# Optimization experiments

Measured on AMD Instinct MI355X. Metric: run time of the kernel, lower is better.

## Reference

```python
import jax, jax.numpy as jnp
import numpy as np

B, T, DIM = 64, 4096, 256
NFILT, KSIZE = 32, 31
PAD = (KSIZE - 1) // 2
NEG = -1e30  # score mask value (finite stand-in for -inf, safe for grads)


def setup_inputs() -> dict:
    key = jax.random.key(0)
    ks = jax.random.split(key, 10)
    query = jax.random.normal(ks[0], (B, DIM), dtype=jnp.float32)
    keys = jax.random.normal(ks[1], (B, T, DIM), dtype=jnp.float32)
    values = jax.random.normal(ks[2], (B, T, DIM), dtype=jnp.float32)
    prev_alignment = jax.random.uniform(ks[3], (B, T), dtype=jnp.float32)
    prev_alignment = prev_alignment / jnp.sum(prev_alignment, axis=1, keepdims=True)
    mask = jax.random.randint(ks[4], (B, T), 0, 2).astype(bool)
    # learned parameters
    Wq = jax.random.normal(ks[5], (DIM, DIM), dtype=jnp.float32) / np.sqrt(DIM)
    conv_w = jax.random.normal(ks[6], (NFILT, 1, KSIZE), dtype=jnp.float32) / np.sqrt(KSIZE)
    Wloc = jax.random.normal(ks[7], (DIM, NFILT), dtype=jnp.float32) / np.sqrt(NFILT)
    v_w = jax.random.normal(ks[8], (1, DIM), dtype=jnp.float32) / np.sqrt(DIM)
    v_b = jnp.zeros((1,), dtype=jnp.float32)
    return {"query": query, "keys": keys, "values": values,
            "prev_alignment": prev_alignment, "mask": mask,
            "Wq": Wq, "conv_w": conv_w, "Wloc": Wloc, "v_w": v_w, "v_b": v_b}


def reference(query, keys, values, prev_alignment, mask, Wq, conv_w, Wloc, v_w, v_b):
    # query projection: (B, dim) -> (B, 1, dim)
    q = (query @ Wq.T)[:, None, :]
    # location conv: (B, 1, T) -> (B, 32, T)
    filters = jax.lax.conv_general_dilated(
        prev_alignment[:, None, :], conv_w,
        window_strides=(1,), padding=[(PAD, PAD)],
        dimension_numbers=("NCH", "OIH", "NCH"))
    # location features: (B, T, dim)
    loc = jnp.einsum("bft,df->btd", filters, Wloc)
    # additive score: v^T tanh(q + loc + keys) -> (B, T)
    align = jnp.einsum("btd,d->bt", jnp.tanh(q + loc + keys), v_w[0]) + v_b[0]
    align = jnp.where(mask, NEG, align)
    align = jax.nn.softmax(align, axis=1)
    # attention context: (B, dim)
    attention = jnp.einsum("bt,btd->bd", align, values)
    return attention, align
```

## Files before the change

### kernel.cpp

```cpp
#include <hip/hip_runtime.h>

#define B_     64
#define T_     4096
#define DIM_   256
#define NFILT_ 32
#define KSIZE_ 31
#define PAD_   15
#define NEG_   -1e30f

__global__ __launch_bounds__(256) void prep_kernel(
    const float* __restrict__ query, const float* __restrict__ Wq,
    const float* __restrict__ conv_w, const float* __restrict__ Wloc,
    float* __restrict__ q_ws, float* __restrict__ M_ws) {
  const int tid = threadIdx.x;
  if (blockIdx.x == 64) {
    __shared__ float cw[NFILT_ * KSIZE_];
    for (int i = tid; i < NFILT_ * KSIZE_; i += 256) cw[i] = conv_w[i];
    __syncthreads();
    const int d = tid;
    float wl[NFILT_];
#pragma unroll
    for (int f = 0; f < NFILT_; ++f) wl[f] = Wloc[d * NFILT_ + f];
#pragma unroll 4
    for (int k = 0; k < KSIZE_; ++k) {
      float acc = 0.f;
#pragma unroll
      for (int f = 0; f < NFILT_; ++f) acc = fmaf(cw[f * KSIZE_ + k], wl[f], acc);
      M_ws[d * KSIZE_ + k] = acc;
    }
  } else {
    const int b = blockIdx.x;
    __shared__ __align__(16) float qrow[DIM_];
    qrow[tid] = query[b * DIM_ + tid];
    __syncthreads();
    const int d = tid;
    const float4* Wq4 = (const float4*)(Wq + (size_t)d * DIM_);
    const float4* q4 = (const float4*)qrow;
    float acc = 0.f;
#pragma unroll 8
    for (int i = 0; i < DIM_ / 4; ++i) {
      float4 w = Wq4[i];
      float4 q = q4[i];
      acc = fmaf(w.x, q.x, acc);
      acc = fmaf(w.y, q.y, acc);
      acc = fmaf(w.z, q.z, acc);
      acc = fmaf(w.w, q.w, acc);
    }
    q_ws[b * DIM_ + d] = acc;
  }
}

__global__ __launch_bounds__(256) void score_kernel(
    const float* __restrict__ keys, const float* __restrict__ prev,
    const int* __restrict__ mask, const float* __restrict__ v_w,
    const float* __restrict__ v_b, const float* __restrict__ q_ws,
    const float* __restrict__ M_ws, float* __restrict__ align_out) {
  const int TC = 256;
  const int chunk = blockIdx.x, b = blockIdx.y;
  const int t0 = chunk * TC;
  const int tid = threadIdx.x;
  const int d = tid;
  const int lane = tid & 63, wave = tid >> 6;

  __shared__ float prevs[TC + 2 * PAD_];
  __shared__ __align__(16) float red[TC * 4];

  for (int i = tid; i < TC + 2 * PAD_; i += 256) {
    int g = t0 - PAD_ + i;
    prevs[i] = (g >= 0 && g < T_) ? prev[(size_t)b * T_ + g] : 0.f;
  }

  float m[KSIZE_];
#pragma unroll
  for (int k = 0; k < KSIZE_; ++k) m[k] = M_ws[d * KSIZE_ + k];
  const float qd = q_ws[b * DIM_ + d];
  const float vwd = v_w[d];
  __syncthreads();

  const float* krow = keys + ((size_t)b * T_ + t0) * DIM_ + d;
#pragma unroll 2
  for (int tl = 0; tl < TC; ++tl) {
    float key = krow[(size_t)tl * DIM_];
    float loc = 0.f;
#pragma unroll
    for (int k = 0; k < KSIZE_; ++k) loc = fmaf(prevs[tl + k], m[k], loc);
    float x = qd + loc + key;
    float e = __expf(2.f * x);
    float th = 1.f - __fdividef(2.f, e + 1.f);
    float c = th * vwd;
#pragma unroll
    for (int off = 32; off > 0; off >>= 1) c += __shfl_xor(c, off, 64);
    if (lane == 0) red[tl * 4 + wave] = c;
  }
  __syncthreads();

  {
    const int tl = tid;
    float4 r = ((const float4*)red)[tl];
    float s = r.x + r.y + r.z + r.w + v_b[0];
    int t = t0 + tl;
    float sc = mask[(size_t)b * T_ + t] ? NEG_ : s;
    align_out[(size_t)b * T_ + t] = sc;
  }
}

__global__ __launch_bounds__(256) void softmax_kernel(float* __restrict__ align) {
  const int b = blockIdx.x, tid = threadIdx.x;
  const int lane = tid & 63, wave = tid >> 6;
  float* row = align + (size_t)b * T_;
  float v[16];
  float mx = -__builtin_inff();
#pragma unroll
  for (int i = 0; i < 16; ++i) {
    v[i] = row[tid + i * 256];
    mx = fmaxf(mx, v[i]);
  }
  __shared__ float redm[4];
  __shared__ float reds[4];
#pragma unroll
  for (int off = 32; off > 0; off >>= 1) mx = fmaxf(mx, __shfl_xor(mx, off, 64));
  if (lane == 0) redm[wave] = mx;
  __syncthreads();
  mx = fmaxf(fmaxf(redm[0], redm[1]), fmaxf(redm[2], redm[3]));
  float s = 0.f;
#pragma unroll
  for (int i = 0; i < 16; ++i) {
    v[i] = __expf(v[i] - mx);
    s += v[i];
  }
#pragma unroll
  for (int off = 32; off > 0; off >>= 1) s += __shfl_xor(s, off, 64);
  if (lane == 0) reds[wave] = s;
  __syncthreads();
  s = reds[0] + reds[1] + reds[2] + reds[3];
  float inv = __fdividef(1.f, s);
#pragma unroll
  for (int i = 0; i < 16; ++i) row[tid + i * 256] = v[i] * inv;
}

__global__ __launch_bounds__(256) void context_kernel(
    const float* __restrict__ values, const float* __restrict__ align,
    float* __restrict__ attn_out) {
  const int TC = 256;
  const int b = blockIdx.y;
  const int t0 = blockIdx.x * TC;
  const int tid = threadIdx.x, lane = tid & 63, wave = tid >> 6;
  float4 acc = make_float4(0.f, 0.f, 0.f, 0.f);
  const float4* vals = (const float4*)values;
  const float* al = align + (size_t)b * T_ + t0;
#pragma unroll 4
  for (int it = 0; it < TC / 4; ++it) {
    int tl = it * 4 + wave;
    float a = al[tl];
    float4 v = vals[((size_t)b * T_ + t0 + tl) * (DIM_ / 4) + lane];
    acc.x = fmaf(a, v.x, acc.x);
    acc.y = fmaf(a, v.y, acc.y);
    acc.z = fmaf(a, v.z, acc.z);
    acc.w = fmaf(a, v.w, acc.w);
  }
  __shared__ __align__(16) float red[4 * DIM_];
  ((float4*)red)[wave * 64 + lane] = acc;
  __syncthreads();
  const int d = tid;
  float s = red[0 * DIM_ + d] + red[1 * DIM_ + d] + red[2 * DIM_ + d] +
            red[3 * DIM_ + d];
  atomicAdd(&attn_out[b * DIM_ + d], s);
}

extern "C" void kernel_launch(void* const* d_in, const int* in_sizes, int n_in,
                              void* d_out, int out_size, void* d_ws,
                              size_t ws_size, hipStream_t stream) {
  const float* query = (const float*)d_in[0];
  const float* keys = (const float*)d_in[1];
  const float* values = (const float*)d_in[2];
  const float* prev = (const float*)d_in[3];
  const int* mask = (const int*)d_in[4];
  const float* Wq = (const float*)d_in[5];
  const float* conv_w = (const float*)d_in[6];
  const float* Wloc = (const float*)d_in[7];
  const float* v_w = (const float*)d_in[8];
  const float* v_b = (const float*)d_in[9];

  float* attn_out = (float*)d_out;
  float* align_out = (float*)d_out + B_ * DIM_;
  float* q_ws = (float*)d_ws;
  float* M_ws = q_ws + B_ * DIM_;

  hipMemsetAsync(attn_out, 0, B_ * DIM_ * sizeof(float), stream);
  prep_kernel<<<65, 256, 0, stream>>>(query, Wq, conv_w, Wloc, q_ws, M_ws);
  score_kernel<<<dim3(16, 64), 256, 0, stream>>>(keys, prev, mask, v_w, v_b,
                                                 q_ws, M_ws, align_out);
  softmax_kernel<<<64, 256, 0, stream>>>(align_out);
  context_kernel<<<dim3(16, 64), 256, 0, stream>>>(values, align_out, attn_out);
}
```

Measured before the change: 666.1 us.

## Skip masked positions in score and context kernels, tile score reduction via LDS

The score kernel now skips loading keys and computing tanh for masked time steps, and prefetches the next key one step ahead. It replaces the per-timestep wave shuffle reduction with tiles of 32 timesteps written to padded shared memory and reduced cooperatively. The context kernel caches alignment weights in shared memory and skips value loads wherever the weight is exactly zero, which covers masked positions after softmax underflow. This targets the memory traffic of keys and values for the roughly half of positions that are masked, at the cost of divergent branches and extra barriers.

```diff
diff --git a/kernel.cpp b/kernel.cpp
--- a/kernel.cpp
+++ b/kernel.cpp
@@ -7,6 +7,9 @@
 #define KSIZE_ 31
 #define PAD_   15
 #define NEG_   -1e30f
+#define TCB_   256
+#define TT_    32
+#define CS_    257
 
 __global__ __launch_bounds__(256) void prep_kernel(
     const float* __restrict__ query, const float* __restrict__ Wq,
@@ -55,52 +58,88 @@
     const int* __restrict__ mask, const float* __restrict__ v_w,
     const float* __restrict__ v_b, const float* __restrict__ q_ws,
     const float* __restrict__ M_ws, float* __restrict__ align_out) {
-  const int TC = 256;
   const int chunk = blockIdx.x, b = blockIdx.y;
-  const int t0 = chunk * TC;
+  const int t0 = chunk * TCB_;
   const int tid = threadIdx.x;
   const int d = tid;
-  const int lane = tid & 63, wave = tid >> 6;
-
-  __shared__ float prevs[TC + 2 * PAD_];
-  __shared__ __align__(16) float red[TC * 4];
-
-  for (int i = tid; i < TC + 2 * PAD_; i += 256) {
+
+  __shared__ float prevs[TCB_ + 2 * PAD_];
+  __shared__ int msk[TCB_];
+  __shared__ float c_s[TT_ * CS_];
+  __shared__ float partial[TT_ * 9];
+
+  for (int i = tid; i < TCB_ + 2 * PAD_; i += 256) {
     int g = t0 - PAD_ + i;
     prevs[i] = (g >= 0 && g < T_) ? prev[(size_t)b * T_ + g] : 0.f;
   }
+  msk[tid] = mask[(size_t)b * T_ + t0 + tid];
 
   float m[KSIZE_];
 #pragma unroll
   for (int k = 0; k < KSIZE_; ++k) m[k] = M_ws[d * KSIZE_ + k];
   const float qd = q_ws[b * DIM_ + d];
   const float vwd = v_w[d];
-  __syncthreads();
-
-  const float* krow = keys + ((size_t)b * T_ + t0) * DIM_ + d;
-#pragma unroll 2
-  for (int tl = 0; tl < TC; ++tl) {
-    float key = krow[(size_t)tl * DIM_];
-    float loc = 0.f;
-#pragma unroll
-    for (int k = 0; k < KSIZE_; ++k) loc = fmaf(prevs[tl + k], m[k], loc);
-    float x = qd + loc + key;
-    float e = __expf(2.f * x);
-    float th = 1.f - __fdividef(2.f, e + 1.f);
-    float c = th * vwd;
-#pragma unroll
-    for (int off = 32; off > 0; off >>= 1) c += __shfl_xor(c, off, 64);
-    if (lane == 0) red[tl * 4 + wave] = c;
-  }
-  __syncthreads();
-
-  {
-    const int tl = tid;
-    float4 r = ((const float4*)red)[tl];
-    float s = r.x + r.y + r.z + r.w + v_b[0];
-    int t = t0 + tl;
-    float sc = mask[(size_t)b * T_ + t] ? NEG_ : s;
-    align_out[(size_t)b * T_ + t] = sc;
+  const float vb = v_b[0];
+  __syncthreads();
+
+  const float* kbase = keys + ((size_t)b * T_ + t0) * DIM_ + d;
+
+  for (int tile = 0; tile < TCB_ / TT_; ++tile) {
+    const int tb = tile * TT_;
+
+    bool skip_n = msk[tb] != 0;
+    float key_n = 0.f;
+    if (!skip_n) key_n = kbase[(size_t)tb * DIM_];
+    for (int tl = 0; tl < TT_; ++tl) {
+      bool skip = skip_n;
+      float key = key_n;
+      if (tl + 1 < TT_) {
+        skip_n = msk[tb + tl + 1] != 0;
+        if (!skip_n) key_n = kbase[(size_t)(tb + tl + 1) * DIM_];
+      }
+      if (!skip) {
+        const float* pw = prevs + tb + tl;
+        float l0 = 0.f, l1 = 0.f, l2 = 0.f, l3 = 0.f;
+#pragma unroll
+        for (int k = 0; k < 28; k += 4) {
+          l0 = fmaf(pw[k], m[k], l0);
+          l1 = fmaf(pw[k + 1], m[k + 1], l1);
+          l2 = fmaf(pw[k + 2], m[k + 2], l2);
+          l3 = fmaf(pw[k + 3], m[k + 3], l3);
+        }
+        l0 = fmaf(pw[28], m[28], l0);
+        l1 = fmaf(pw[29], m[29], l1);
+        l2 = fmaf(pw[30], m[30], l2);
+        float x = qd + (l0 + l1) + (l2 + l3) + key;
+        float e = __expf(2.f * x);
+        float th = 1.f - __fdividef(2.f, e + 1.f);
+        c_s[tl * CS_ + d] = th * vwd;
+      }
+    }
+    __syncthreads();
+
+    {
+      const int t = tid & 31, part = tid >> 5;
+      const float* row = c_s + t * CS_ + part * 32;
+      float s0 = 0.f, s1 = 0.f, s2 = 0.f, s3 = 0.f;
+#pragma unroll
+      for (int j = 0; j < 32; j += 4) {
+        s0 += row[j];
+        s1 += row[j + 1];
+        s2 += row[j + 2];
+        s3 += row[j + 3];
+      }
+      partial[t * 9 + part] = (s0 + s1) + (s2 + s3);
+    }
+    __syncthreads();
+
+    if (tid < TT_) {
+      const float* pr = partial + tid * 9;
+      float s = ((pr[0] + pr[1]) + (pr[2] + pr[3])) +
+                ((pr[4] + pr[5]) + (pr[6] + pr[7]));
+      int t = t0 + tb + tid;
+      align_out[(size_t)b * T_ + t] = msk[tb + tid] ? NEG_ : (s + vb);
+    }
   }
 }
 
@@ -145,26 +184,32 @@
   const int b = blockIdx.y;
   const int t0 = blockIdx.x * TC;
   const int tid = threadIdx.x, lane = tid & 63, wave = tid >> 6;
+
+  __shared__ float als[TC];
+  als[tid] = align[(size_t)b * T_ + t0 + tid];
+  __syncthreads();
+
   float4 acc = make_float4(0.f, 0.f, 0.f, 0.f);
-  const float4* vals = (const float4*)values;
-  const float* al = align + (size_t)b * T_ + t0;
-#pragma unroll 4
-  for (int it = 0; it < TC / 4; ++it) {
-    int tl = it * 4 + wave;
-    float a = al[tl];
-    float4 v = vals[((size_t)b * T_ + t0 + tl) * (DIM_ / 4) + lane];
-    acc.x = fmaf(a, v.x, acc.x);
-    acc.y = fmaf(a, v.y, acc.y);
-    acc.z = fmaf(a, v.z, acc.z);
-    acc.w = fmaf(a, v.w, acc.w);
+  const float4* vals = (const float4*)(values + ((size_t)b * T_ + t0) * DIM_);
+#pragma unroll 2
+  for (int j = 0; j < 64; ++j) {
+    int tl = wave * 64 + j;
+    float a = als[tl];
+    if (a != 0.f) {
+      float4 v = vals[(size_t)tl * (DIM_ / 4) + lane];
+      acc.x = fmaf(a, v.x, acc.x);
+      acc.y = fmaf(a, v.y, acc.y);
+      acc.z = fmaf(a, v.z, acc.z);
+      acc.w = fmaf(a, v.w, acc.w);
+    }
   }
   __shared__ __align__(16) float red[4 * DIM_];
   ((float4*)red)[wave * 64 + lane] = acc;
   __syncthreads();
-  const int d = tid;
-  float s = red[0 * DIM_ + d] + red[1 * DIM_ + d] + red[2 * DIM_ + d] +
-            red[3 * DIM_ + d];
-  atomicAdd(&attn_out[b * DIM_ + d], s);
+  const int dd = tid;
+  float s = red[0 * DIM_ + dd] + red[1 * DIM_ + dd] + red[2 * DIM_ + dd] +
+            red[3 * DIM_ + dd];
+  atomicAdd(&attn_out[b * DIM_ + dd], s);
 }
 
 extern "C" void kernel_launch(void* const* d_in, const int* in_sizes, int n_in,
```

New measurement: 571.0 us. -14.3%, faster.
